# Performance work log

Hardware: AMD Instinct MI355X
Metric: run time of the kernel (lower is better)

The kernel has to match this reference:

```python
import jax, jax.numpy as jnp
import numpy as np

H = 16  # num_heads


def setup_inputs() -> dict:
    key = jax.random.key(0)
    ks = jax.random.split(key, 9)
    L, N, E, I = 2048, 2, 2048, 2048
    s = 0.02
    return {
        "query": jax.random.normal(ks[0], (L, N, E), jnp.float32),
        "q_proj": jax.random.normal(ks[1], (I, E), jnp.float32) * s,
        "q_bias": jax.random.normal(ks[2], (I,), jnp.float32) * s,
        "k_proj": jax.random.normal(ks[3], (I, E), jnp.float32) * s,
        "k_bias": jax.random.normal(ks[4], (I,), jnp.float32) * s,
        "v_proj": jax.random.normal(ks[5], (I, E), jnp.float32) * s,
        "v_bias": jax.random.normal(ks[6], (I,), jnp.float32) * s,
        "out_proj": jax.random.normal(ks[7], (E, I), jnp.float32) * s,
        "out_bias": jax.random.normal(ks[8], (E,), jnp.float32) * s,
    }


def reference(query, q_proj, q_bias, k_proj, k_bias, v_proj, v_bias, out_proj, out_bias):
    L, N, E = query.shape
    h = H
    d = q_proj.shape[0] // h
    scale = d ** (-0.5)

    def split_heads(x):
        # [L, N, h*d] -> [N, h, L, d]  (matches view(L, N*h, d).transpose(0,1))
        return x.reshape(L, N, h, d).transpose(1, 2, 0, 3)

    q = split_heads(query @ q_proj.T + q_bias) * scale
    k = split_heads(query @ k_proj.T + k_bias)
    v = split_heads(query @ v_proj.T + v_bias)

    scores = jnp.einsum('nhld,nhkd->nhlk', q, k)  # [N, h, L, L]
    causal = jnp.tril(jnp.ones((L, L), dtype=bool))
    scores = jnp.where(causal, scores, jnp.float32(-10000.0))
    attn = jax.nn.softmax(scores, axis=-1)
    # dropout_p = 0.0 -> identity
    ctx = jnp.einsum('nhlk,nhkd->nhld', attn, v)
    ctx = ctx.transpose(2, 0, 1, 3).reshape(L, N, h * d)  # [L, N, h*d]
    return ctx @ out_proj.T + out_bias  # [L, N, E]
```

## Files before the change

### kernel.cpp

```cpp
#include <hip/hip_runtime.h>
#include <stdint.h>

#define L_SEQ 2048
#define NB 2
#define EMB 2048
#define II 2048
#define NH 16
#define DH 128
#define MROWS (L_SEQ * NB)

typedef __attribute__((ext_vector_type(8))) short bf16x8;
typedef __attribute__((ext_vector_type(4))) float f32x4;
typedef unsigned short u16;
typedef unsigned int u32;

__device__ __forceinline__ u16 f2bf(float f) {
  u32 u = __builtin_bit_cast(u32, f);
  u = u + 0x7fffu + ((u >> 16) & 1u);
  return (u16)(u >> 16);
}
__device__ __forceinline__ u16 f2bf_trunc(float f) {
  return (u16)(__builtin_bit_cast(u32, f) >> 16);
}

__device__ __forceinline__ void gl_lds16(const void* g, const u16* l) {
  __builtin_amdgcn_global_load_lds(
      (const __attribute__((address_space(1))) void*)(uintptr_t)g,
      (__attribute__((address_space(3))) void*)(u32)(uintptr_t)l, 16, 0, 0);
}

__global__ __launch_bounds__(256) void cast_f32_bf16(const float* __restrict__ in,
                                                     u16* __restrict__ out, int n4) {
  int i = blockIdx.x * 256 + threadIdx.x;
  if (i < n4) {
    float4 v = ((const float4*)in)[i];
    ushort4 o;
    o.x = f2bf(v.x); o.y = f2bf(v.y); o.z = f2bf(v.z); o.w = f2bf(v.w);
    ((ushort4*)out)[i] = o;
  }
}

__global__ __launch_bounds__(256) void transpose_v(const u16* __restrict__ V,
                                                   u16* __restrict__ Vt) {
  __shared__ u16 tile[128][72];
  const int lb = blockIdx.x * 64;
  const int h = blockIdx.y;
  const u16* src = V + (size_t)h * L_SEQ * DH;
  u16* dst = Vt + (size_t)h * DH * L_SEQ;
  const int t = threadIdx.x;
  {
    const int l = t & 63, d0 = (t >> 6) * 32;
#pragma unroll
    for (int c = 0; c < 4; c++) {
      uint4 u = *(const uint4*)(src + (size_t)(lb + l) * DH + d0 + c * 8);
      const u16* e = (const u16*)&u;
#pragma unroll
      for (int x = 0; x < 8; x++) tile[d0 + c * 8 + x][l] = e[x];
    }
  }
  __syncthreads();
  {
    const int d = t >> 1, lc = (t & 1) * 32;
#pragma unroll
    for (int c = 0; c < 4; c++) {
      uint4 u = *(const uint4*)&tile[d][lc + c * 8];
      *(uint4*)(dst + (size_t)d * L_SEQ + lb + lc + c * 8) = u;
    }
  }
}

__global__ __launch_bounds__(256) void gemm_nt(
    const u16* __restrict__ A, const u16* __restrict__ B, const float* __restrict__ b0,
    const float* __restrict__ b1, const float* __restrict__ b2, u16* __restrict__ out_bf,
    float* __restrict__ out_f, int Nd, int K, float qscale, int mode) {
  __shared__ __align__(16) u16 a_sm[128 * 32];
  __shared__ __align__(16) u16 b_sm[128 * 32];
  const int t = threadIdx.x;
  const int lane = t & 63, wv = t >> 6;
  const int quad = lane >> 4, l15 = lane & 15;
  const int wm = (wv >> 1) * 64, wn = (wv & 1) * 64;
  const int m0 = blockIdx.y * 128, n0 = blockIdx.x * 128;
  const int sr = lane >> 2;
  const int sc = (lane & 3) * 8;

  f32x4 acc[4][4] = {};
  const u16* abase = A + (size_t)m0 * K;
  const u16* bbase = B + (size_t)n0 * K;

  for (int k0 = 0; k0 < K; k0 += 32) {
    __syncthreads();
#pragma unroll
    for (int j = 0; j < 2; j++) {
      int qi = wv * 2 + j;
      gl_lds16(abase + (size_t)(qi * 16 + sr) * K + k0 + sc, a_sm + qi * 512);
      gl_lds16(bbase + (size_t)(qi * 16 + sr) * K + k0 + sc, b_sm + qi * 512);
    }
    __syncthreads();
    bf16x8 af[4], bfr[4];
#pragma unroll
    for (int i = 0; i < 4; i++)
      af[i] = *(const bf16x8*)(a_sm + (wm + i * 16 + l15) * 32 + quad * 8);
#pragma unroll
    for (int j = 0; j < 4; j++)
      bfr[j] = *(const bf16x8*)(b_sm + (wn + j * 16 + l15) * 32 + quad * 8);
#pragma unroll
    for (int i = 0; i < 4; i++)
#pragma unroll
      for (int j = 0; j < 4; j++)
        acc[i][j] = __builtin_amdgcn_mfma_f32_16x16x32_bf16(af[i], bfr[j], acc[i][j], 0, 0, 0);
  }

  const int mat = n0 >> 11;
  const float* bp = (mode == 1) ? b0 : (mat == 0 ? b0 : (mat == 1 ? b1 : b2));
  const float sc2 = (mode == 0 && mat == 0) ? qscale : 1.0f;
#pragma unroll
  for (int i = 0; i < 4; i++) {
#pragma unroll
    for (int j = 0; j < 4; j++) {
#pragma unroll
      for (int r = 0; r < 4; r++) {
        int row = m0 + wm + i * 16 + quad * 4 + r;
        int col = n0 + wn + j * 16 + l15;
        if (mode == 0) {
          int cc = col & 2047;
          float v = (acc[i][j][r] + bp[cc]) * sc2;
          int l = row >> 1, nb = row & 1;
          int hh = cc >> 7, dd = cc & 127;
          out_bf[(size_t)mat * MROWS * II + ((size_t)(nb * NH + hh) * L_SEQ + l) * DH + dd] =
              f2bf(v);
        } else {
          out_f[(size_t)row * Nd + col] = acc[i][j][r] + bp[col];
        }
      }
    }
  }
}

__global__ __launch_bounds__(128, 2) void flash_attn(
    const u16* __restrict__ Qh, const u16* __restrict__ Kh, const u16* __restrict__ Vt,
    u16* __restrict__ ctx) {
  __shared__ __align__(16) u16 k_sm[64 * 128];
  __shared__ __align__(16) u16 v_sm[128 * 64];
  __shared__ __align__(16) u16 p_sm[2][32 * 64];
  const int bx = blockIdx.x;
  const int nh = ((bx & 7) << 2) | ((bx >> 3) & 3);
  const int qt = 31 - (bx >> 5);
  const int q0 = qt * 64;
  const int nK = qt + 1;
  const int t = threadIdx.x;
  const int lane = t & 63, wv = t >> 6;
  const int quad = lane >> 4, l15 = lane & 15;
  const size_t hq = (size_t)nh * L_SEQ * DH;
  const u16* qp = Qh + hq;
  const u16* kp = Kh + hq;
  const u16* vp = Vt + hq;
  const int n = nh >> 4, h = nh & 15;
  const int krow4 = lane >> 4, kpos = lane & 15;
  const int vrow8 = lane >> 3, vpos = lane & 7;
  const int x7 = l15 & 7;
  u16* pw = (u16*)p_sm[wv];

  bf16x8 qf[2][4];
#pragma unroll
  for (int mi = 0; mi < 2; mi++)
#pragma unroll
    for (int ks = 0; ks < 4; ks++)
      qf[mi][ks] = *(const bf16x8*)(qp + (size_t)(q0 + wv * 32 + mi * 16 + l15) * DH +
                                    ks * 32 + quad * 8);

  f32x4 o_acc[2][8] = {};
  float l_part[2][4] = {};

#pragma unroll 1
  for (int jb = 0; jb < nK; jb++) {
    const int kb = jb * 64;
    __syncthreads();
#pragma unroll
    for (int i = 0; i < 8; i++) {
      int ci = wv * 8 + i;
      int kr = ci * 4 + krow4;
      gl_lds16(kp + (size_t)(kb + kr) * DH + (kpos ^ (kr & 7)) * 8, k_sm + ci * 512);
      int vd = ci * 8 + vrow8;
      gl_lds16(vp + (size_t)vd * L_SEQ + kb + (vpos ^ (vd & 7)) * 8, v_sm + ci * 512);
    }
    __syncthreads();

    f32x4 s[2][4] = {};
#pragma unroll
    for (int nt = 0; nt < 4; nt++) {
#pragma unroll
      for (int ks = 0; ks < 4; ks++) {
        bf16x8 kf = *(const bf16x8*)(k_sm + (nt * 16 + l15) * 128 + ((ks * 4 + quad) ^ x7) * 8);
#pragma unroll
        for (int mi = 0; mi < 2; mi++)
          s[mi][nt] = __builtin_amdgcn_mfma_f32_16x16x32_bf16(qf[mi][ks], kf, s[mi][nt], 0, 0, 0);
      }
    }

    const bool diag = (jb == nK - 1);
#pragma unroll
    for (int mi = 0; mi < 2; mi++) {
      const int rowg = q0 + wv * 32 + mi * 16 + quad * 4;
#pragma unroll
      for (int nt = 0; nt < 4; nt++) {
        const int colg = kb + nt * 16 + l15;
#pragma unroll
        for (int r = 0; r < 4; r++) {
          float p = __builtin_amdgcn_exp2f(s[mi][nt][r]);
          if (diag && colg > rowg + r) p = 0.f;
          l_part[mi][r] += p;
          int prow = mi * 16 + quad * 4 + r;
          int pos = (nt * 2 + (l15 >> 3)) ^ (prow & 7);
          pw[prow * 64 + pos * 8 + (l15 & 7)] = f2bf_trunc(p);
        }
      }
    }
    __asm__ volatile("s_waitcnt lgkmcnt(0)" ::: "memory");

    bf16x8 pf[2][2];
#pragma unroll
    for (int mi = 0; mi < 2; mi++)
#pragma unroll
      for (int ks = 0; ks < 2; ks++)
        pf[mi][ks] =
            *(const bf16x8*)(pw + (mi * 16 + l15) * 64 + ((ks * 4 + quad) ^ x7) * 8);
#pragma unroll
    for (int nt = 0; nt < 8; nt++) {
#pragma unroll
      for (int ks = 0; ks < 2; ks++) {
        bf16x8 vf = *(const bf16x8*)(v_sm + (nt * 16 + l15) * 64 + ((ks * 4 + quad) ^ x7) * 8);
#pragma unroll
        for (int mi = 0; mi < 2; mi++)
          o_acc[mi][nt] =
              __builtin_amdgcn_mfma_f32_16x16x32_bf16(pf[mi][ks], vf, o_acc[mi][nt], 0, 0, 0);
      }
    }
  }

#pragma unroll
  for (int mi = 0; mi < 2; mi++) {
#pragma unroll
    for (int r = 0; r < 4; r++) {
      float lv = l_part[mi][r];
#pragma unroll
      for (int off = 1; off < 16; off <<= 1) lv += __shfl_xor(lv, off, 64);
      float inv = 1.f / lv;
      const int lrow = q0 + wv * 32 + mi * 16 + quad * 4 + r;
#pragma unroll
      for (int nt = 0; nt < 8; nt++) {
        int dd = nt * 16 + l15;
        ctx[((size_t)lrow * NB + n) * EMB + h * DH + dd] = f2bf(o_acc[mi][nt][r] * inv);
      }
    }
  }
}

extern "C" void kernel_launch(void* const* d_in, const int* in_sizes, int n_in,
                              void* d_out, int out_size, void* d_ws, size_t ws_size,
                              hipStream_t stream) {
  const float* query    = (const float*)d_in[0];
  const float* q_proj   = (const float*)d_in[1];
  const float* q_bias   = (const float*)d_in[2];
  const float* k_proj   = (const float*)d_in[3];
  const float* k_bias   = (const float*)d_in[4];
  const float* v_proj   = (const float*)d_in[5];
  const float* v_bias   = (const float*)d_in[6];
  const float* out_proj = (const float*)d_in[7];
  const float* out_bias = (const float*)d_in[8];

  u16* ws  = (u16*)d_ws;
  u16* Xbf = ws;
  u16* Wq  = Xbf + (size_t)MROWS * EMB;
  u16* Wk  = Wq + (size_t)II * EMB;
  u16* Wv  = Wk + (size_t)II * EMB;
  u16* Wo  = Wv + (size_t)II * EMB;
  u16* Qw  = Wo + (size_t)EMB * II;
  u16* Kw  = Qw + (size_t)MROWS * II;
  u16* Vw  = Kw + (size_t)MROWS * II;
  u16* Cw  = Vw + (size_t)MROWS * II;
  u16* Vtb = Xbf;

  int nq4 = MROWS * EMB / 4;
  int nw4 = II * EMB / 4;
  cast_f32_bf16<<<nq4 / 256, 256, 0, stream>>>(query, Xbf, nq4);
  cast_f32_bf16<<<nw4 / 256, 256, 0, stream>>>(q_proj, Wq, nw4);
  cast_f32_bf16<<<nw4 / 256, 256, 0, stream>>>(k_proj, Wk, nw4);
  cast_f32_bf16<<<nw4 / 256, 256, 0, stream>>>(v_proj, Wv, nw4);
  cast_f32_bf16<<<nw4 / 256, 256, 0, stream>>>(out_proj, Wo, nw4);

  const float qscale = 0.08838834764831845f * 1.4426950408889634f;
  gemm_nt<<<dim3(3 * II / 128, MROWS / 128), 256, 0, stream>>>(
      Xbf, Wq, q_bias, k_bias, v_bias, Qw, nullptr, 3 * II, EMB, qscale, 0);

  transpose_v<<<dim3(L_SEQ / 64, NB * NH), 256, 0, stream>>>(Vw, Vtb);

  flash_attn<<<1024, 128, 0, stream>>>(Qw, Kw, Vtb, Cw);

  gemm_nt<<<dim3(EMB / 128, MROWS / 128), 256, 0, stream>>>(
      Cw, Wo, out_bias, nullptr, nullptr, nullptr, (float*)d_out, EMB, II, 1.0f, 1);
}
```

Before: 447.0 us.

## Enlarge attention and GEMM tiles, swizzle GEMM LDS, fuse cast kernels

Flash attention now uses 256-thread blocks over 128x128 query/key tiles, reusing the K LDS buffer for P after a barrier and pairing heavy/light causal tiles across the grid. The projection GEMM loads a 64-deep K slice per iteration with an XOR-swizzled LDS layout, halving barriers and reducing bank conflicts. The five cast launches are merged into one kernel. Larger tiles raise register and LDS pressure and may reduce occupancy, and the extra barrier in attention adds synchronisation.

```diff
diff --git a/kernel.cpp b/kernel.cpp
--- a/kernel.cpp
+++ b/kernel.cpp
@@ -29,15 +29,27 @@
       (__attribute__((address_space(3))) void*)(u32)(uintptr_t)l, 16, 0, 0);
 }
 
-__global__ __launch_bounds__(256) void cast_f32_bf16(const float* __restrict__ in,
-                                                     u16* __restrict__ out, int n4) {
-  int i = blockIdx.x * 256 + threadIdx.x;
-  if (i < n4) {
-    float4 v = ((const float4*)in)[i];
-    ushort4 o;
-    o.x = f2bf(v.x); o.y = f2bf(v.y); o.z = f2bf(v.z); o.w = f2bf(v.w);
-    ((ushort4*)out)[i] = o;
-  }
+__global__ __launch_bounds__(256) void cast_all(
+    const float* __restrict__ q, const float* __restrict__ w0, const float* __restrict__ w1,
+    const float* __restrict__ w2, const float* __restrict__ w3, u16* __restrict__ dq,
+    u16* __restrict__ dw) {
+  const int b = blockIdx.x, t = threadIdx.x;
+  const float* src;
+  u16* dst;
+  int idx;
+  if (b < 8192) {
+    src = q; dst = dq; idx = b * 256 + t;
+  } else {
+    int u = b - 8192;
+    int sel = u >> 12;
+    src = (sel == 0) ? w0 : (sel == 1) ? w1 : (sel == 2) ? w2 : w3;
+    dst = dw + (size_t)sel * II * EMB;
+    idx = (u & 4095) * 256 + t;
+  }
+  float4 v = ((const float4*)src)[idx];
+  ushort4 o;
+  o.x = f2bf(v.x); o.y = f2bf(v.y); o.z = f2bf(v.z); o.w = f2bf(v.w);
+  ((ushort4*)dst)[idx] = o;
 }
 
 __global__ __launch_bounds__(256) void transpose_v(const u16* __restrict__ V,
@@ -73,41 +85,46 @@
     const u16* __restrict__ A, const u16* __restrict__ B, const float* __restrict__ b0,
     const float* __restrict__ b1, const float* __restrict__ b2, u16* __restrict__ out_bf,
     float* __restrict__ out_f, int Nd, int K, float qscale, int mode) {
-  __shared__ __align__(16) u16 a_sm[128 * 32];
-  __shared__ __align__(16) u16 b_sm[128 * 32];
+  __shared__ __align__(16) u16 a_sm[128 * 64];
+  __shared__ __align__(16) u16 b_sm[128 * 64];
   const int t = threadIdx.x;
   const int lane = t & 63, wv = t >> 6;
   const int quad = lane >> 4, l15 = lane & 15;
+  const int x7 = l15 & 7;
   const int wm = (wv >> 1) * 64, wn = (wv & 1) * 64;
   const int m0 = blockIdx.y * 128, n0 = blockIdx.x * 128;
-  const int sr = lane >> 2;
-  const int sc = (lane & 3) * 8;
+  const int srow = lane >> 3;
+  const int schunk = (lane & 7) ^ (lane >> 3);
 
   f32x4 acc[4][4] = {};
   const u16* abase = A + (size_t)m0 * K;
   const u16* bbase = B + (size_t)n0 * K;
 
-  for (int k0 = 0; k0 < K; k0 += 32) {
-    __syncthreads();
-#pragma unroll
-    for (int j = 0; j < 2; j++) {
-      int qi = wv * 2 + j;
-      gl_lds16(abase + (size_t)(qi * 16 + sr) * K + k0 + sc, a_sm + qi * 512);
-      gl_lds16(bbase + (size_t)(qi * 16 + sr) * K + k0 + sc, b_sm + qi * 512);
-    }
-    __syncthreads();
-    bf16x8 af[4], bfr[4];
-#pragma unroll
-    for (int i = 0; i < 4; i++)
-      af[i] = *(const bf16x8*)(a_sm + (wm + i * 16 + l15) * 32 + quad * 8);
-#pragma unroll
-    for (int j = 0; j < 4; j++)
-      bfr[j] = *(const bf16x8*)(b_sm + (wn + j * 16 + l15) * 32 + quad * 8);
-#pragma unroll
-    for (int i = 0; i < 4; i++)
+  for (int k0 = 0; k0 < K; k0 += 64) {
+    __syncthreads();
+#pragma unroll
+    for (int j = 0; j < 4; j++) {
+      int ci = wv * 4 + j;
+      int row = ci * 8 + srow;
+      gl_lds16(abase + (size_t)row * K + k0 + schunk * 8, a_sm + ci * 512);
+      gl_lds16(bbase + (size_t)row * K + k0 + schunk * 8, b_sm + ci * 512);
+    }
+    __syncthreads();
+#pragma unroll
+    for (int ks = 0; ks < 2; ks++) {
+      bf16x8 af[4], bfr[4];
+#pragma unroll
+      for (int i = 0; i < 4; i++)
+        af[i] = *(const bf16x8*)(a_sm + (wm + i * 16 + l15) * 64 + ((ks * 4 + quad) ^ x7) * 8);
 #pragma unroll
       for (int j = 0; j < 4; j++)
-        acc[i][j] = __builtin_amdgcn_mfma_f32_16x16x32_bf16(af[i], bfr[j], acc[i][j], 0, 0, 0);
+        bfr[j] = *(const bf16x8*)(b_sm + (wn + j * 16 + l15) * 64 + ((ks * 4 + quad) ^ x7) * 8);
+#pragma unroll
+      for (int i = 0; i < 4; i++)
+#pragma unroll
+        for (int j = 0; j < 4; j++)
+          acc[i][j] = __builtin_amdgcn_mfma_f32_16x16x32_bf16(af[i], bfr[j], acc[i][j], 0, 0, 0);
+    }
   }
 
   const int mat = n0 >> 11;
@@ -136,29 +153,29 @@
   }
 }
 
-__global__ __launch_bounds__(128, 2) void flash_attn(
+__global__ __launch_bounds__(256, 2) void flash_attn(
     const u16* __restrict__ Qh, const u16* __restrict__ Kh, const u16* __restrict__ Vt,
     u16* __restrict__ ctx) {
-  __shared__ __align__(16) u16 k_sm[64 * 128];
-  __shared__ __align__(16) u16 v_sm[128 * 64];
-  __shared__ __align__(16) u16 p_sm[2][32 * 64];
+  __shared__ __align__(16) u16 k_sm[128 * 128];
+  __shared__ __align__(16) u16 v_sm[128 * 128];
   const int bx = blockIdx.x;
   const int nh = ((bx & 7) << 2) | ((bx >> 3) & 3);
-  const int qt = 31 - (bx >> 5);
-  const int q0 = qt * 64;
+  const int g = (bx >> 5) & 7;
+  const int qt = (bx < 256) ? (15 - g) : g;
+  const int q0 = qt * 128;
   const int nK = qt + 1;
   const int t = threadIdx.x;
   const int lane = t & 63, wv = t >> 6;
   const int quad = lane >> 4, l15 = lane & 15;
+  const int x7 = l15 & 7;
   const size_t hq = (size_t)nh * L_SEQ * DH;
   const u16* qp = Qh + hq;
   const u16* kp = Kh + hq;
   const u16* vp = Vt + hq;
   const int n = nh >> 4, h = nh & 15;
-  const int krow4 = lane >> 4, kpos = lane & 15;
-  const int vrow8 = lane >> 3, vpos = lane & 7;
-  const int x7 = l15 & 7;
-  u16* pw = (u16*)p_sm[wv];
+  const int srow = lane >> 4;
+  const int spos = lane & 15;
+  u16* pw = k_sm + wv * 4096;
 
   bf16x8 qf[2][4];
 #pragma unroll
@@ -173,21 +190,21 @@
 
 #pragma unroll 1
   for (int jb = 0; jb < nK; jb++) {
-    const int kb = jb * 64;
+    const int kb = jb * 128;
     __syncthreads();
 #pragma unroll
     for (int i = 0; i < 8; i++) {
       int ci = wv * 8 + i;
-      int kr = ci * 4 + krow4;
-      gl_lds16(kp + (size_t)(kb + kr) * DH + (kpos ^ (kr & 7)) * 8, k_sm + ci * 512);
-      int vd = ci * 8 + vrow8;
-      gl_lds16(vp + (size_t)vd * L_SEQ + kb + (vpos ^ (vd & 7)) * 8, v_sm + ci * 512);
-    }
-    __syncthreads();
-
-    f32x4 s[2][4] = {};
-#pragma unroll
-    for (int nt = 0; nt < 4; nt++) {
+      int row = ci * 4 + srow;
+      int gc = spos ^ (row & 7);
+      gl_lds16(kp + (size_t)(kb + row) * DH + gc * 8, k_sm + ci * 512);
+      gl_lds16(vp + (size_t)row * L_SEQ + kb + gc * 8, v_sm + ci * 512);
+    }
+    __syncthreads();
+
+    f32x4 s[2][8] = {};
+#pragma unroll
+    for (int nt = 0; nt < 8; nt++) {
 #pragma unroll
       for (int ks = 0; ks < 4; ks++) {
         bf16x8 kf = *(const bf16x8*)(k_sm + (nt * 16 + l15) * 128 + ((ks * 4 + quad) ^ x7) * 8);
@@ -196,39 +213,40 @@
           s[mi][nt] = __builtin_amdgcn_mfma_f32_16x16x32_bf16(qf[mi][ks], kf, s[mi][nt], 0, 0, 0);
       }
     }
-
-    const bool diag = (jb == nK - 1);
+    __syncthreads();
+
+    const bool diag = (jb == qt);
 #pragma unroll
     for (int mi = 0; mi < 2; mi++) {
       const int rowg = q0 + wv * 32 + mi * 16 + quad * 4;
 #pragma unroll
-      for (int nt = 0; nt < 4; nt++) {
+      for (int nt = 0; nt < 8; nt++) {
         const int colg = kb + nt * 16 + l15;
 #pragma unroll
         for (int r = 0; r < 4; r++) {
           float p = __builtin_amdgcn_exp2f(s[mi][nt][r]);
           if (diag && colg > rowg + r) p = 0.f;
           l_part[mi][r] += p;
-          int prow = mi * 16 + quad * 4 + r;
-          int pos = (nt * 2 + (l15 >> 3)) ^ (prow & 7);
-          pw[prow * 64 + pos * 8 + (l15 & 7)] = f2bf_trunc(p);
+          int pr = mi * 16 + quad * 4 + r;
+          int chunk = nt * 2 + (l15 >> 3);
+          int pos = chunk ^ (pr & 7);
+          pw[pr * 128 + pos * 8 + (l15 & 7)] = f2bf_trunc(p);
         }
       }
     }
     __asm__ volatile("s_waitcnt lgkmcnt(0)" ::: "memory");
 
-    bf16x8 pf[2][2];
+    bf16x8 pf[2][4];
 #pragma unroll
     for (int mi = 0; mi < 2; mi++)
 #pragma unroll
-      for (int ks = 0; ks < 2; ks++)
-        pf[mi][ks] =
-            *(const bf16x8*)(pw + (mi * 16 + l15) * 64 + ((ks * 4 + quad) ^ x7) * 8);
+      for (int ks = 0; ks < 4; ks++)
+        pf[mi][ks] = *(const bf16x8*)(pw + (mi * 16 + l15) * 128 + ((ks * 4 + quad) ^ x7) * 8);
 #pragma unroll
     for (int nt = 0; nt < 8; nt++) {
 #pragma unroll
-      for (int ks = 0; ks < 2; ks++) {
-        bf16x8 vf = *(const bf16x8*)(v_sm + (nt * 16 + l15) * 64 + ((ks * 4 + quad) ^ x7) * 8);
+      for (int ks = 0; ks < 4; ks++) {
+        bf16x8 vf = *(const bf16x8*)(v_sm + (nt * 16 + l15) * 128 + ((ks * 4 + quad) ^ x7) * 8);
 #pragma unroll
         for (int mi = 0; mi < 2; mi++)
           o_acc[mi][nt] =
@@ -280,13 +298,8 @@
   u16* Cw  = Vw + (size_t)MROWS * II;
   u16* Vtb = Xbf;
 
-  int nq4 = MROWS * EMB / 4;
-  int nw4 = II * EMB / 4;
-  cast_f32_bf16<<<nq4 / 256, 256, 0, stream>>>(query, Xbf, nq4);
-  cast_f32_bf16<<<nw4 / 256, 256, 0, stream>>>(q_proj, Wq, nw4);
-  cast_f32_bf16<<<nw4 / 256, 256, 0, stream>>>(k_proj, Wk, nw4);
-  cast_f32_bf16<<<nw4 / 256, 256, 0, stream>>>(v_proj, Wv, nw4);
-  cast_f32_bf16<<<nw4 / 256, 256, 0, stream>>>(out_proj, Wo, nw4);
+  cast_all<<<8192 + 4 * 4096, 256, 0, stream>>>(query, q_proj, k_proj, v_proj, out_proj,
+                                                Xbf, Wq);
 
   const float qscale = 0.08838834764831845f * 1.4426950408889634f;
   gemm_nt<<<dim3(3 * II / 128, MROWS / 128), 256, 0, stream>>>(
@@ -294,7 +307,7 @@
 
   transpose_v<<<dim3(L_SEQ / 64, NB * NH), 256, 0, stream>>>(Vw, Vtb);
 
-  flash_attn<<<1024, 128, 0, stream>>>(Qw, Kw, Vtb, Cw);
+  flash_attn<<<512, 256, 0, stream>>>(Qw, Kw, Vtb, Cw);
 
   gemm_nt<<<dim3(EMB / 128, MROWS / 128), 256, 0, stream>>>(
       Cw, Wo, out_bias, nullptr, nullptr, nullptr, (float*)d_out, EMB, II, 1.0f, 1);
```

Result: no change. 443.4 us (-0.8%).
